# Performance work log

Hardware: AMD Instinct MI355X
Metric: run time of the kernel (lower is better)

Reference implementation:

```python
import jax, jax.numpy as jnp
import numpy as np

B, IN_DIM, EMBED_DIM, NUM_TOKENS, CODEBOOK = 4096, 1024, 128, 16, 1024
HID = 512
LATENT = EMBED_DIM * NUM_TOKENS  # 2048


def _lin_init(key, fan_in, fan_out):
    # torch nn.Linear default: U(-1/sqrt(fan_in), 1/sqrt(fan_in))
    kw, kb = jax.random.split(key)
    bound = 1.0 / np.sqrt(fan_in)
    W = jax.random.uniform(kw, (fan_in, fan_out), jnp.float32, -bound, bound)
    b = jax.random.uniform(kb, (fan_out,), jnp.float32, -bound, bound)
    return W, b


def setup_inputs() -> dict:
    key = jax.random.key(0)
    ks = jax.random.split(key, 8)
    x = jax.random.normal(ks[0], (B, IN_DIM), jnp.float32)
    eW1, eb1 = _lin_init(ks[1], IN_DIM, HID)
    eW2, eb2 = _lin_init(ks[2], HID, HID)
    eW3, eb3 = _lin_init(ks[3], HID, LATENT)
    dW1, db1 = _lin_init(ks[4], LATENT, HID)
    dW2, db2 = _lin_init(ks[5], HID, HID)
    dW3, db3 = _lin_init(ks[6], HID, IN_DIM)
    codebook = jax.random.normal(ks[7], (CODEBOOK, EMBED_DIM), jnp.float32)
    return dict(x=x, eW1=eW1, eb1=eb1, eW2=eW2, eb2=eb2, eW3=eW3, eb3=eb3,
                dW1=dW1, db1=db1, dW2=dW2, db2=db2, dW3=dW3, db3=db3,
                codebook=codebook)


def reference(x, eW1, eb1, eW2, eb2, eW3, eb3,
              dW1, db1, dW2, db2, dW3, db3, codebook):
    gelu = lambda t: jax.nn.gelu(t, approximate=False)  # torch GELU is exact
    # encoder MLP
    h = gelu(x @ eW1 + eb1)
    h = gelu(h @ eW2 + eb2)
    z = h @ eW3 + eb3                         # [B, num_tokens*embed_dim]
    z = z.reshape(B * NUM_TOKENS, EMBED_DIM)  # (...) h d flattened
    # VQ: euclidean nearest codebook entry (||z||^2 constant for argmin)
    dist = -2.0 * (z @ codebook.T) + jnp.sum(codebook * codebook, axis=-1)  # [B*T, K]
    indices = jnp.argmin(dist, axis=-1)       # [B*T] int
    quantized = codebook[indices]             # gather [B*T, D]
    commit_loss = jnp.mean((jax.lax.stop_gradient(quantized) - z) ** 2)
    # straight-through estimator
    q = z + jax.lax.stop_gradient(quantized - z)
    q = q.reshape(B, LATENT)
    # decoder MLP
    h = gelu(q @ dW1 + db1)
    h = gelu(h @ dW2 + db2)
    rec = h @ dW3 + db3                       # [B, in_dim]
    return rec, indices.reshape(B, NUM_TOKENS), commit_loss
```

## Files before the change

kernel.cpp:

```cpp
#include <hip/hip_runtime.h>
#include <hip/hip_bf16.h>
#include <math.h>

#define BDIM   4096
#define IN_DIM 1024
#define HID    512
#define LAT    2048
#define EMB    128
#define NCODE  1024
#define NROWS  65536
#define OUT_REC  (4096 * 1024)
#define OUT_IDX  (OUT_REC)
#define OUT_LOSS (OUT_REC + 65536)

#define H1_OFF    0u
#define H2_OFF    (2u*1024*1024)
#define Z_OFF     (4u*1024*1024)
#define CBT_OFF   (12u*1024*1024)
#define CNORM_OFF (CBT_OFF + 131072u)
#define LACC_OFF  (CNORM_OFF + 1024u)
#define WT_OFF    (LACC_OFF + 8u)

typedef __attribute__((ext_vector_type(8))) __bf16 bf16x8;
typedef __attribute__((ext_vector_type(4))) float f32x4;
typedef __attribute__((ext_vector_type(8))) unsigned short u16x8;

__device__ __forceinline__ float gelu_exact(float x) {
    return 0.5f * x * (1.0f + erff(x * 0.7071067811865476f));
}

__device__ __forceinline__ void split_bf16(float v, unsigned short& hi, unsigned short& lo) {
    __hip_bfloat16 h = __float2bfloat16(v);
    float hf = __bfloat162float(h);
    __hip_bfloat16 l = __float2bfloat16(v - hf);
    hi = *reinterpret_cast<unsigned short*>(&h);
    lo = *reinterpret_cast<unsigned short*>(&l);
}

template<bool GELU>
__global__ __launch_bounds__(256) void gemm32_kernel(
    const float* __restrict__ A, const float* __restrict__ W,
    const float* __restrict__ bias, float* __restrict__ C,
    int M, int N, int K)
{
    __shared__ float As[32][132];
    __shared__ float Ws[32][64];
    const int tid = threadIdx.x;
    const int tx = tid & 15, ty = tid >> 4;
    const int bm = blockIdx.x * 128, bn = blockIdx.y * 64;

    const int a_row = tid >> 3;
    const int a_kq  = (tid & 7) * 4;
    const int w_kr  = tid >> 4;
    const int w_n4  = (tid & 15) * 4;

    float acc[8][4] = {};

    for (int k0 = 0; k0 < K; k0 += 32) {
        float4 av[4], wv[2];
        #pragma unroll
        for (int p = 0; p < 4; ++p)
            av[p] = *reinterpret_cast<const float4*>(&A[(size_t)(bm + a_row + p * 32) * K + k0 + a_kq]);
        #pragma unroll
        for (int p = 0; p < 2; ++p)
            wv[p] = *reinterpret_cast<const float4*>(&W[(size_t)(k0 + w_kr + p * 16) * N + bn + w_n4]);
        __syncthreads();
        #pragma unroll
        for (int p = 0; p < 4; ++p) {
            As[a_kq + 0][a_row + p * 32] = av[p].x;
            As[a_kq + 1][a_row + p * 32] = av[p].y;
            As[a_kq + 2][a_row + p * 32] = av[p].z;
            As[a_kq + 3][a_row + p * 32] = av[p].w;
        }
        #pragma unroll
        for (int p = 0; p < 2; ++p)
            *reinterpret_cast<float4*>(&Ws[w_kr + p * 16][w_n4]) = wv[p];
        __syncthreads();

        #pragma unroll
        for (int kk = 0; kk < 32; ++kk) {
            f32x4 a0 = *reinterpret_cast<const f32x4*>(&As[kk][ty * 8]);
            f32x4 a1 = *reinterpret_cast<const f32x4*>(&As[kk][ty * 8 + 4]);
            f32x4 w4 = *reinterpret_cast<const f32x4*>(&Ws[kk][tx * 4]);
            float a[8] = {a0.x, a0.y, a0.z, a0.w, a1.x, a1.y, a1.z, a1.w};
            float w[4] = {w4.x, w4.y, w4.z, w4.w};
            #pragma unroll
            for (int i = 0; i < 8; ++i)
                #pragma unroll
                for (int j = 0; j < 4; ++j)
                    acc[i][j] = fmaf(a[i], w[j], acc[i][j]);
        }
    }

    #pragma unroll
    for (int i = 0; i < 8; ++i) {
        const int row = bm + ty * 8 + i;
        float4 o;
        float* op = reinterpret_cast<float*>(&o);
        #pragma unroll
        for (int j = 0; j < 4; ++j) {
            float v = acc[i][j] + bias[bn + tx * 4 + j];
            if (GELU) v = gelu_exact(v);
            op[j] = v;
        }
        *reinterpret_cast<float4*>(&C[(size_t)row * N + bn + tx * 4]) = o;
    }
}

__global__ __launch_bounds__(128) void cnorm_kernel(const float* __restrict__ cb,
                                                    float* __restrict__ cnorm) {
    const int c = blockIdx.x;
    float v = cb[(size_t)c * EMB + threadIdx.x];
    float s = v * v;
    #pragma unroll
    for (int off = 32; off > 0; off >>= 1) s += __shfl_down(s, off, 64);
    __shared__ float ps[2];
    if ((threadIdx.x & 63) == 0) ps[threadIdx.x >> 6] = s;
    __syncthreads();
    if (threadIdx.x == 0) cnorm[c] = ps[0] + ps[1];
}

__global__ __launch_bounds__(256) void transpose_f32_kernel(const float* __restrict__ in,
        float* __restrict__ out, int R, int C) {
    __shared__ float tile[32][33];
    const int r0 = blockIdx.y * 32, c0 = blockIdx.x * 32;
    const int tx = threadIdx.x, ty = threadIdx.y;
    #pragma unroll
    for (int i = 0; i < 4; ++i)
        tile[ty * 4 + i][tx] = in[(size_t)(r0 + ty * 4 + i) * C + c0 + tx];
    __syncthreads();
    #pragma unroll
    for (int i = 0; i < 4; ++i)
        out[(size_t)(c0 + ty * 4 + i) * R + r0 + tx] = tile[tx][ty * 4 + i];
}

__global__ __launch_bounds__(256) void wsplitT_kernel(const float* __restrict__ W,
        unsigned short* __restrict__ hiT, unsigned short* __restrict__ loT, int K, int N) {
    __shared__ float tile[32][33];
    const int k0 = blockIdx.y * 32, n0 = blockIdx.x * 32;
    const int tx = threadIdx.x, ty = threadIdx.y;
    #pragma unroll
    for (int i = 0; i < 4; ++i)
        tile[ty * 4 + i][tx] = W[(size_t)(k0 + ty * 4 + i) * N + n0 + tx];
    __syncthreads();
    #pragma unroll
    for (int i = 0; i < 4; ++i) {
        float v = tile[tx][ty * 4 + i];
        unsigned short h, l; split_bf16(v, h, l);
        size_t o = (size_t)(n0 + ty * 4 + i) * K + k0 + tx;
        hiT[o] = h; loT[o] = l;
    }
}

__global__ __launch_bounds__(256) void vq3_kernel(
    const float* __restrict__ Z, unsigned short* __restrict__ qpack,
    const float* __restrict__ cbT, const float* __restrict__ cb,
    const float* __restrict__ cnorm,
    float* __restrict__ idx_out, float* __restrict__ loss_accum)
{
    __shared__ float Zs[128][68];
    __shared__ float Cs[32][260];
    __shared__ int bidx_s[64];
    __shared__ float lred[4];
    const int tid = threadIdx.x;
    const int tx = tid & 31, ty = tid >> 5;
    const int r0 = blockIdx.x * 64;

    #pragma unroll
    for (int p = 0; p < 8; ++p) {
        int s = tid + p * 256;
        int row = s >> 5, k4 = (s & 31) * 4;
        float4 v = *reinterpret_cast<const float4*>(&Z[(size_t)(r0 + row) * EMB + k4]);
        Zs[k4 + 0][row] = v.x; Zs[k4 + 1][row] = v.y;
        Zs[k4 + 2][row] = v.z; Zs[k4 + 3][row] = v.w;
    }

    float best[8]; int bidx[8];
    #pragma unroll
    for (int i = 0; i < 8; ++i) { best[i] = 3.4e38f; bidx[i] = 0; }

    for (int cc = 0; cc < 4; ++cc) {
        float acc[8][8] = {};
        for (int kc = 0; kc < 4; ++kc) {
            __syncthreads();
            #pragma unroll
            for (int p = 0; p < 8; ++p) {
                int s = tid + p * 256;
                int kr = s >> 6, c4 = (s & 63) * 4;
                float4 v = *reinterpret_cast<const float4*>(
                    &cbT[(size_t)(kc * 32 + kr) * NCODE + cc * 256 + c4]);
                *reinterpret_cast<float4*>(&Cs[kr][c4]) = v;
            }
            __syncthreads();
            #pragma unroll
            for (int kk = 0; kk < 32; ++kk) {
                f32x4 a0 = *reinterpret_cast<const f32x4*>(&Zs[kc * 32 + kk][ty * 8]);
                f32x4 a1 = *reinterpret_cast<const f32x4*>(&Zs[kc * 32 + kk][ty * 8 + 4]);
                f32x4 c0 = *reinterpret_cast<const f32x4*>(&Cs[kk][tx * 4]);
                f32x4 c1 = *reinterpret_cast<const f32x4*>(&Cs[kk][128 + tx * 4]);
                float a[8] = {a0.x, a0.y, a0.z, a0.w, a1.x, a1.y, a1.z, a1.w};
                float c[8] = {c0.x, c0.y, c0.z, c0.w, c1.x, c1.y, c1.z, c1.w};
                #pragma unroll
                for (int i = 0; i < 8; ++i)
                    #pragma unroll
                    for (int j = 0; j < 8; ++j)
                        acc[i][j] = fmaf(a[i], c[j], acc[i][j]);
            }
        }
        #pragma unroll
        for (int j = 0; j < 8; ++j) {
            int c = cc * 256 + ((j < 4) ? (tx * 4 + j) : (128 + tx * 4 + (j - 4)));
            float cn = cnorm[c];
            #pragma unroll
            for (int i = 0; i < 8; ++i) {
                float d = cn - 2.0f * acc[i][j];
                if (d < best[i]) { best[i] = d; bidx[i] = c; }
            }
        }
    }
    #pragma unroll
    for (int i = 0; i < 8; ++i) {
        float bd = best[i]; int bi = bidx[i];
        #pragma unroll
        for (int m = 1; m < 32; m <<= 1) {
            float od = __shfl_xor(bd, m); int oi = __shfl_xor(bi, m);
            if (od < bd || (od == bd && oi < bi)) { bd = od; bi = oi; }
        }
        if (tx == 0) {
            int row = ty * 8 + i;
            idx_out[r0 + row] = (float)bi;
            bidx_s[row] = bi;
        }
    }
    __syncthreads();
    float lsum = 0.0f;
    #pragma unroll
    for (int p = 0; p < 32; ++p) {
        int el = p * 256 + tid;
        int row = el >> 7, k = el & 127;
        int bi = bidx_s[row];
        float qv = cb[(size_t)bi * EMB + k];
        float zv = Zs[k][row];
        float dv = qv - zv;
        lsum += dv * dv;
        unsigned short h, l; split_bf16(qv, h, l);
        size_t base = (size_t)(r0 + row) * 256;
        qpack[base + k] = h;
        qpack[base + 128 + k] = l;
    }
    #pragma unroll
    for (int off = 32; off > 0; off >>= 1) lsum += __shfl_down(lsum, off, 64);
    if ((tid & 63) == 0) lred[tid >> 6] = lsum;
    __syncthreads();
    if (tid == 0) atomicAdd(loss_accum, lred[0] + lred[1] + lred[2] + lred[3]);
}

template<int AMODE, bool GELU, int OMODE>
__global__ __launch_bounds__(256) void mfma_gemm_kernel(
    const unsigned short* __restrict__ Ahi, const unsigned short* __restrict__ Alo,
    const unsigned short* __restrict__ BThi, const unsigned short* __restrict__ BTlo,
    const float* __restrict__ bias,
    float* __restrict__ Cf, unsigned short* __restrict__ Ohi, unsigned short* __restrict__ Olo,
    int M, int N, int K)
{
    __shared__ unsigned short AsH[128][40], AsL[128][40], BsH[128][40], BsL[128][40];
    const int tid = threadIdx.x;
    const int lane = tid & 63, wid = tid >> 6;
    const int wm = (wid >> 1) * 64, wn = (wid & 1) * 64;
    const int m0 = blockIdx.x * 128, n0 = blockIdx.y * 128;

    f32x4 acc[4][4];
    #pragma unroll
    for (int i = 0; i < 4; ++i)
        #pragma unroll
        for (int j = 0; j < 4; ++j)
            acc[i][j] = f32x4{0.f, 0.f, 0.f, 0.f};

    const int s0 = tid, s1 = tid + 256;
    const int r0_ = s0 >> 2, k0_ = (s0 & 3) * 8;
    const int r1_ = s1 >> 2, k1_ = (s1 & 3) * 8;

    for (int k0 = 0; k0 < K; k0 += 32) {
        u16x8 vA0, vA1, vAl0, vAl1, vB0, vB1, vBl0, vBl1;
        if (AMODE == 1) {
            int kk0 = k0 + k0_, kk1 = k0 + k1_;
            size_t g0 = ((size_t)(m0 + r0_) * 16 + (kk0 >> 7)) * 256 + (kk0 & 127);
            size_t g1 = ((size_t)(m0 + r1_) * 16 + (kk1 >> 7)) * 256 + (kk1 & 127);
            vA0  = *reinterpret_cast<const u16x8*>(Ahi + g0);
            vAl0 = *reinterpret_cast<const u16x8*>(Ahi + g0 + 128);
            vA1  = *reinterpret_cast<const u16x8*>(Ahi + g1);
            vAl1 = *reinterpret_cast<const u16x8*>(Ahi + g1 + 128);
        } else {
            size_t g0 = (size_t)(m0 + r0_) * K + k0 + k0_;
            size_t g1 = (size_t)(m0 + r1_) * K + k0 + k1_;
            vA0  = *reinterpret_cast<const u16x8*>(Ahi + g0);
            vAl0 = *reinterpret_cast<const u16x8*>(Alo + g0);
            vA1  = *reinterpret_cast<const u16x8*>(Ahi + g1);
            vAl1 = *reinterpret_cast<const u16x8*>(Alo + g1);
        }
        {
            size_t g0 = (size_t)(n0 + r0_) * K + k0 + k0_;
            size_t g1 = (size_t)(n0 + r1_) * K + k0 + k1_;
            vB0  = *reinterpret_cast<const u16x8*>(BThi + g0);
            vBl0 = *reinterpret_cast<const u16x8*>(BTlo + g0);
            vB1  = *reinterpret_cast<const u16x8*>(BThi + g1);
            vBl1 = *reinterpret_cast<const u16x8*>(BTlo + g1);
        }
        __syncthreads();
        *reinterpret_cast<u16x8*>(&AsH[r0_][k0_]) = vA0;
        *reinterpret_cast<u16x8*>(&AsH[r1_][k1_]) = vA1;
        *reinterpret_cast<u16x8*>(&AsL[r0_][k0_]) = vAl0;
        *reinterpret_cast<u16x8*>(&AsL[r1_][k1_]) = vAl1;
        *reinterpret_cast<u16x8*>(&BsH[r0_][k0_]) = vB0;
        *reinterpret_cast<u16x8*>(&BsH[r1_][k1_]) = vB1;
        *reinterpret_cast<u16x8*>(&BsL[r0_][k0_]) = vBl0;
        *reinterpret_cast<u16x8*>(&BsL[r1_][k1_]) = vBl1;
        __syncthreads();

        const int fr = lane & 15, fk = (lane >> 4) * 8;
        bf16x8 ah[4], al[4];
        #pragma unroll
        for (int mi = 0; mi < 4; ++mi) {
            ah[mi] = *reinterpret_cast<const bf16x8*>(&AsH[wm + mi * 16 + fr][fk]);
            al[mi] = *reinterpret_cast<const bf16x8*>(&AsL[wm + mi * 16 + fr][fk]);
        }
        #pragma unroll
        for (int ni = 0; ni < 4; ++ni) {
            bf16x8 bh = *reinterpret_cast<const bf16x8*>(&BsH[wn + ni * 16 + fr][fk]);
            bf16x8 bl = *reinterpret_cast<const bf16x8*>(&BsL[wn + ni * 16 + fr][fk]);
            #pragma unroll
            for (int mi = 0; mi < 4; ++mi) {
                acc[mi][ni] = __builtin_amdgcn_mfma_f32_16x16x32_bf16(ah[mi], bh, acc[mi][ni], 0, 0, 0);
                acc[mi][ni] = __builtin_amdgcn_mfma_f32_16x16x32_bf16(ah[mi], bl, acc[mi][ni], 0, 0, 0);
                acc[mi][ni] = __builtin_amdgcn_mfma_f32_16x16x32_bf16(al[mi], bh, acc[mi][ni], 0, 0, 0);
            }
        }
    }

    const int fr = lane & 15, fq = lane >> 4;
    #pragma unroll
    for (int ni = 0; ni < 4; ++ni) {
        int col = n0 + wn + ni * 16 + fr;
        float bv = bias[col];
        #pragma unroll
        for (int mi = 0; mi < 4; ++mi) {
            #pragma unroll
            for (int r = 0; r < 4; ++r) {
                int row = m0 + wm + mi * 16 + fq * 4 + r;
                float v = acc[mi][ni][r] + bv;
                if (GELU) v = gelu_exact(v);
                if (OMODE == 0) {
                    Cf[(size_t)row * N + col] = v;
                } else {
                    unsigned short h, l; split_bf16(v, h, l);
                    Ohi[(size_t)row * N + col] = h;
                    Olo[(size_t)row * N + col] = l;
                }
            }
        }
    }
}

__global__ void loss_fin_kernel(const float* __restrict__ acc, float* __restrict__ out) {
    out[0] = acc[0] * (1.0f / 8388608.0f);
}

extern "C" void kernel_launch(void* const* d_in, const int* in_sizes, int n_in,
                              void* d_out, int out_size, void* d_ws, size_t ws_size,
                              hipStream_t stream) {
    const float* x   = (const float*)d_in[0];
    const float* eW1 = (const float*)d_in[1];
    const float* eb1 = (const float*)d_in[2];
    const float* eW2 = (const float*)d_in[3];
    const float* eb2 = (const float*)d_in[4];
    const float* eW3 = (const float*)d_in[5];
    const float* eb3 = (const float*)d_in[6];
    const float* dW1 = (const float*)d_in[7];
    const float* db1 = (const float*)d_in[8];
    const float* dW2 = (const float*)d_in[9];
    const float* db2 = (const float*)d_in[10];
    const float* dW3 = (const float*)d_in[11];
    const float* db3 = (const float*)d_in[12];
    const float* cb  = (const float*)d_in[13];

    float* out = (float*)d_out;
    float* ws  = (float*)d_ws;

    float* h1    = ws + H1_OFF;
    float* h2    = ws + H2_OFF;
    float* z     = ws + Z_OFF;
    float* cbT   = ws + CBT_OFF;
    float* cnorm = ws + CNORM_OFF;
    float* lacc  = ws + LACC_OFF;

    unsigned short* qpack = (unsigned short*)z;
    unsigned short* h1hi = (unsigned short*)h1;
    unsigned short* h1lo = (unsigned short*)(h1 + 1048576);
    unsigned short* h2hi = (unsigned short*)h2;
    unsigned short* h2lo = (unsigned short*)(h2 + 1048576);
    unsigned short* wt   = (unsigned short*)(ws + WT_OFF);
    unsigned short* W1TH = wt;
    unsigned short* W1TL = wt + 1048576u;
    unsigned short* W2TH = wt + 2097152u;
    unsigned short* W2TL = wt + 2359296u;
    unsigned short* W3TH = wt + 2621440u;
    unsigned short* W3TL = wt + 3145728u;

    hipMemsetAsync(lacc, 0, sizeof(float), stream);
    cnorm_kernel<<<NCODE, 128, 0, stream>>>(cb, cnorm);
    transpose_f32_kernel<<<dim3(EMB / 32, NCODE / 32), dim3(32, 8), 0, stream>>>(cb, cbT, NCODE, EMB);
    wsplitT_kernel<<<dim3(HID / 32, LAT / 32),    dim3(32, 8), 0, stream>>>(dW1, W1TH, W1TL, LAT, HID);
    wsplitT_kernel<<<dim3(HID / 32, HID / 32),    dim3(32, 8), 0, stream>>>(dW2, W2TH, W2TL, HID, HID);
    wsplitT_kernel<<<dim3(IN_DIM / 32, HID / 32), dim3(32, 8), 0, stream>>>(dW3, W3TH, W3TL, HID, IN_DIM);

    gemm32_kernel<true ><<<dim3(BDIM / 128, HID / 64), 256, 0, stream>>>(x,  eW1, eb1, h1, BDIM, HID, IN_DIM);
    gemm32_kernel<true ><<<dim3(BDIM / 128, HID / 64), 256, 0, stream>>>(h1, eW2, eb2, h2, BDIM, HID, HID);
    gemm32_kernel<false><<<dim3(BDIM / 128, LAT / 64), 256, 0, stream>>>(h2, eW3, eb3, z,  BDIM, LAT, HID);

    vq3_kernel<<<NROWS / 64, 256, 0, stream>>>(z, qpack, cbT, cb, cnorm, out + OUT_IDX, lacc);

    mfma_gemm_kernel<1, true, 1><<<dim3(BDIM / 128, HID / 128), 256, 0, stream>>>(
        qpack, nullptr, W1TH, W1TL, db1, nullptr, h1hi, h1lo, BDIM, HID, LAT);
    mfma_gemm_kernel<0, true, 1><<<dim3(BDIM / 128, HID / 128), 256, 0, stream>>>(
        h1hi, h1lo, W2TH, W2TL, db2, nullptr, h2hi, h2lo, BDIM, HID, HID);
    mfma_gemm_kernel<0, false, 0><<<dim3(BDIM / 128, IN_DIM / 128), 256, 0, stream>>>(
        h2hi, h2lo, W3TH, W3TL, db3, out, nullptr, nullptr, BDIM, IN_DIM, HID);

    loss_fin_kernel<<<1, 1, 0, stream>>>(lacc, out + OUT_LOSS);
}
```

Measured before the change: 841.7 us.

## Retile encoder FP32 GEMMs to 8x8 per-thread and fix LDS transpose stores

The encoder FP32 GEMM now computes an 8x8 register tile per thread in 128-thread blocks with a 64x128 output tile and K-step 16, replacing the 8x4 tile in 256-thread blocks. Each thread does more FMAs per LDS read. The A-tile and the VQ Z-tile loads now gather four rows per column with scalar global loads so the shared-memory transposed writes become float4 stores instead of four scattered scalar stores. The trade-off is more accumulator registers and less coalesced global reads for A and Z.

```diff
diff --git a/kernel.cpp b/kernel.cpp
--- a/kernel.cpp
+++ b/kernel.cpp
@@ -38,56 +38,64 @@
 }
 
 template<bool GELU>
-__global__ __launch_bounds__(256) void gemm32_kernel(
+__global__ __launch_bounds__(128) void gemm8x8_kernel(
     const float* __restrict__ A, const float* __restrict__ W,
     const float* __restrict__ bias, float* __restrict__ C,
     int M, int N, int K)
 {
-    __shared__ float As[32][132];
-    __shared__ float Ws[32][64];
+    __shared__ float As[16][68];
+    __shared__ float Ws[16][132];
     const int tid = threadIdx.x;
     const int tx = tid & 15, ty = tid >> 4;
-    const int bm = blockIdx.x * 128, bn = blockIdx.y * 64;
-
-    const int a_row = tid >> 3;
-    const int a_kq  = (tid & 7) * 4;
-    const int w_kr  = tid >> 4;
-    const int w_n4  = (tid & 15) * 4;
-
-    float acc[8][4] = {};
-
-    for (int k0 = 0; k0 < K; k0 += 32) {
-        float4 av[4], wv[2];
-        #pragma unroll
-        for (int p = 0; p < 4; ++p)
-            av[p] = *reinterpret_cast<const float4*>(&A[(size_t)(bm + a_row + p * 32) * K + k0 + a_kq]);
-        #pragma unroll
-        for (int p = 0; p < 2; ++p)
-            wv[p] = *reinterpret_cast<const float4*>(&W[(size_t)(k0 + w_kr + p * 16) * N + bn + w_n4]);
+    const int bm = blockIdx.x * 64, bn = blockIdx.y * 128;
+
+    float acc[8][8] = {};
+
+    for (int k0 = 0; k0 < K; k0 += 16) {
+        float4 ag[2];
+        #pragma unroll
+        for (int p = 0; p < 2; ++p) {
+            const int s = tid + 128 * p;
+            const int k = s & 15, mg = s >> 4;
+            ag[p].x = A[(size_t)(bm + mg * 4 + 0) * K + k0 + k];
+            ag[p].y = A[(size_t)(bm + mg * 4 + 1) * K + k0 + k];
+            ag[p].z = A[(size_t)(bm + mg * 4 + 2) * K + k0 + k];
+            ag[p].w = A[(size_t)(bm + mg * 4 + 3) * K + k0 + k];
+        }
+        float4 wg[4];
+        #pragma unroll
+        for (int p = 0; p < 4; ++p) {
+            const int s = tid + 128 * p;
+            const int kw = s >> 5, ng = s & 31;
+            wg[p] = *reinterpret_cast<const float4*>(&W[(size_t)(k0 + kw) * N + bn + ng * 4]);
+        }
         __syncthreads();
         #pragma unroll
+        for (int p = 0; p < 2; ++p) {
+            const int s = tid + 128 * p;
+            const int k = s & 15, mg = s >> 4;
+            *reinterpret_cast<float4*>(&As[k][mg * 4]) = ag[p];
+        }
+        #pragma unroll
         for (int p = 0; p < 4; ++p) {
-            As[a_kq + 0][a_row + p * 32] = av[p].x;
-            As[a_kq + 1][a_row + p * 32] = av[p].y;
-            As[a_kq + 2][a_row + p * 32] = av[p].z;
-            As[a_kq + 3][a_row + p * 32] = av[p].w;
-        }
-        #pragma unroll
-        for (int p = 0; p < 2; ++p)
-            *reinterpret_cast<float4*>(&Ws[w_kr + p * 16][w_n4]) = wv[p];
+            const int s = tid + 128 * p;
+            const int kw = s >> 5, ng = s & 31;
+            *reinterpret_cast<float4*>(&Ws[kw][ng * 4]) = wg[p];
+        }
         __syncthreads();
 
         #pragma unroll
-        for (int kk = 0; kk < 32; ++kk) {
+        for (int kk = 0; kk < 16; ++kk) {
             f32x4 a0 = *reinterpret_cast<const f32x4*>(&As[kk][ty * 8]);
             f32x4 a1 = *reinterpret_cast<const f32x4*>(&As[kk][ty * 8 + 4]);
-            f32x4 w4 = *reinterpret_cast<const f32x4*>(&Ws[kk][tx * 4]);
+            f32x4 w0 = *reinterpret_cast<const f32x4*>(&Ws[kk][tx * 8]);
+            f32x4 w1 = *reinterpret_cast<const f32x4*>(&Ws[kk][tx * 8 + 4]);
             float a[8] = {a0.x, a0.y, a0.z, a0.w, a1.x, a1.y, a1.z, a1.w};
-            float w[4] = {w4.x, w4.y, w4.z, w4.w};
+            float w[8] = {w0.x, w0.y, w0.z, w0.w, w1.x, w1.y, w1.z, w1.w};
             #pragma unroll
             for (int i = 0; i < 8; ++i)
                 #pragma unroll
-                for (int j = 0; j < 4; ++j)
+                for (int j = 0; j < 8; ++j)
                     acc[i][j] = fmaf(a[i], w[j], acc[i][j]);
         }
     }
@@ -95,15 +103,18 @@
     #pragma unroll
     for (int i = 0; i < 8; ++i) {
         const int row = bm + ty * 8 + i;
-        float4 o;
-        float* op = reinterpret_cast<float*>(&o);
-        #pragma unroll
-        for (int j = 0; j < 4; ++j) {
-            float v = acc[i][j] + bias[bn + tx * 4 + j];
-            if (GELU) v = gelu_exact(v);
-            op[j] = v;
-        }
-        *reinterpret_cast<float4*>(&C[(size_t)row * N + bn + tx * 4]) = o;
+        #pragma unroll
+        for (int h = 0; h < 2; ++h) {
+            float4 o;
+            float* op = reinterpret_cast<float*>(&o);
+            #pragma unroll
+            for (int j = 0; j < 4; ++j) {
+                float v = acc[i][h * 4 + j] + bias[bn + tx * 8 + h * 4 + j];
+                if (GELU) v = gelu_exact(v);
+                op[j] = v;
+            }
+            *reinterpret_cast<float4*>(&C[(size_t)row * N + bn + tx * 8 + h * 4]) = o;
+        }
     }
 }
 
@@ -152,7 +163,7 @@
     }
 }
 
-__global__ __launch_bounds__(256) void vq3_kernel(
+__global__ __launch_bounds__(256) void vq4_kernel(
     const float* __restrict__ Z, unsigned short* __restrict__ qpack,
     const float* __restrict__ cbT, const float* __restrict__ cb,
     const float* __restrict__ cnorm,
@@ -168,11 +179,14 @@
 
     #pragma unroll
     for (int p = 0; p < 8; ++p) {
-        int s = tid + p * 256;
-        int row = s >> 5, k4 = (s & 31) * 4;
-        float4 v = *reinterpret_cast<const float4*>(&Z[(size_t)(r0 + row) * EMB + k4]);
-        Zs[k4 + 0][row] = v.x; Zs[k4 + 1][row] = v.y;
-        Zs[k4 + 2][row] = v.z; Zs[k4 + 3][row] = v.w;
+        const int s = tid + p * 256;
+        const int k = s & 127, rg = s >> 7;
+        float4 v;
+        v.x = Z[(size_t)(r0 + rg * 4 + 0) * EMB + k];
+        v.y = Z[(size_t)(r0 + rg * 4 + 1) * EMB + k];
+        v.z = Z[(size_t)(r0 + rg * 4 + 2) * EMB + k];
+        v.w = Z[(size_t)(r0 + rg * 4 + 3) * EMB + k];
+        *reinterpret_cast<float4*>(&Zs[k][rg * 4]) = v;
     }
 
     float best[8]; int bidx[8];
@@ -185,8 +199,8 @@
             __syncthreads();
             #pragma unroll
             for (int p = 0; p < 8; ++p) {
-                int s = tid + p * 256;
-                int kr = s >> 6, c4 = (s & 63) * 4;
+                const int s = tid + p * 256;
+                const int kr = s >> 6, c4 = (s & 63) * 4;
                 float4 v = *reinterpret_cast<const float4*>(
                     &cbT[(size_t)(kc * 32 + kr) * NCODE + cc * 256 + c4]);
                 *reinterpret_cast<float4*>(&Cs[kr][c4]) = v;
@@ -209,11 +223,11 @@
         }
         #pragma unroll
         for (int j = 0; j < 8; ++j) {
-            int c = cc * 256 + ((j < 4) ? (tx * 4 + j) : (128 + tx * 4 + (j - 4)));
-            float cn = cnorm[c];
+            const int c = cc * 256 + ((j < 4) ? (tx * 4 + j) : (128 + tx * 4 + (j - 4)));
+            const float cn = cnorm[c];
             #pragma unroll
             for (int i = 0; i < 8; ++i) {
-                float d = cn - 2.0f * acc[i][j];
+                const float d = cn - 2.0f * acc[i][j];
                 if (d < best[i]) { best[i] = d; bidx[i] = c; }
             }
         }
@@ -227,7 +241,7 @@
             if (od < bd || (od == bd && oi < bi)) { bd = od; bi = oi; }
         }
         if (tx == 0) {
-            int row = ty * 8 + i;
+            const int row = ty * 8 + i;
             idx_out[r0 + row] = (float)bi;
             bidx_s[row] = bi;
         }
@@ -236,15 +250,15 @@
     float lsum = 0.0f;
     #pragma unroll
     for (int p = 0; p < 32; ++p) {
-        int el = p * 256 + tid;
-        int row = el >> 7, k = el & 127;
-        int bi = bidx_s[row];
-        float qv = cb[(size_t)bi * EMB + k];
-        float zv = Zs[k][row];
-        float dv = qv - zv;
+        const int el = p * 256 + tid;
+        const int row = el >> 7, k = el & 127;
+        const int bi = bidx_s[row];
+        const float qv = cb[(size_t)bi * EMB + k];
+        const float zv = Zs[k][row];
+        const float dv = qv - zv;
         lsum += dv * dv;
         unsigned short h, l; split_bf16(qv, h, l);
-        size_t base = (size_t)(r0 + row) * 256;
+        const size_t base = (size_t)(r0 + row) * 256;
         qpack[base + k] = h;
         qpack[base + 128 + k] = l;
     }
@@ -413,11 +427,11 @@
     wsplitT_kernel<<<dim3(HID / 32, HID / 32),    dim3(32, 8), 0, stream>>>(dW2, W2TH, W2TL, HID, HID);
     wsplitT_kernel<<<dim3(IN_DIM / 32, HID / 32), dim3(32, 8), 0, stream>>>(dW3, W3TH, W3TL, HID, IN_DIM);
 
-    gemm32_kernel<true ><<<dim3(BDIM / 128, HID / 64), 256, 0, stream>>>(x,  eW1, eb1, h1, BDIM, HID, IN_DIM);
-    gemm32_kernel<true ><<<dim3(BDIM / 128, HID / 64), 256, 0, stream>>>(h1, eW2, eb2, h2, BDIM, HID, HID);
-    gemm32_kernel<false><<<dim3(BDIM / 128, LAT / 64), 256, 0, stream>>>(h2, eW3, eb3, z,  BDIM, LAT, HID);
-
-    vq3_kernel<<<NROWS / 64, 256, 0, stream>>>(z, qpack, cbT, cb, cnorm, out + OUT_IDX, lacc);
+    gemm8x8_kernel<true ><<<dim3(BDIM / 64, HID / 128), 128, 0, stream>>>(x,  eW1, eb1, h1, BDIM, HID, IN_DIM);
+    gemm8x8_kernel<true ><<<dim3(BDIM / 64, HID / 128), 128, 0, stream>>>(h1, eW2, eb2, h2, BDIM, HID, HID);
+    gemm8x8_kernel<false><<<dim3(BDIM / 64, LAT / 128), 128, 0, stream>>>(h2, eW3, eb3, z,  BDIM, LAT, HID);
+
+    vq4_kernel<<<NROWS / 64, 256, 0, stream>>>(z, qpack, cbT, cb, cnorm, out + OUT_IDX, lacc);
 
     mfma_gemm_kernel<1, true, 1><<<dim3(BDIM / 128, HID / 128), 256, 0, stream>>>(
         qpack, nullptr, W1TH, W1TL, db1, nullptr, h1hi, h1lo, BDIM, HID, LAT);
```

New measurement: 1.056 ms. 25.5% more time.
